# Optimization experiments

Hardware: AMD Instinct MI355X
Metric: run time of the kernel (lower is better)

Reference implementation:

```python
import jax, jax.numpy as jnp
import numpy as np

NUM_CLASSES = 8192
FEAT_DIM = 256
BATCH = 1024
TEMPERATURE = 0.1
BASE_TEMPERATURE = 0.1
PROTO_M = 0.5
EPS = 1e-12  # F.normalize eps


def setup_inputs() -> dict:
    key = jax.random.key(0)
    k1, k2, k3 = jax.random.split(key, 3)
    features = jax.random.normal(k1, (BATCH, FEAT_DIM), dtype=jnp.float32)
    proto = jax.random.normal(k2, (NUM_CLASSES, FEAT_DIM), dtype=jnp.float32)
    # prototypes buffer is unit-normalized after init_class_prototypes
    proto = proto / jnp.maximum(jnp.linalg.norm(proto, axis=1, keepdims=True), EPS)
    labels = jax.random.randint(k3, (BATCH,), 0, NUM_CLASSES, dtype=jnp.int64)
    return {"features": features, "prototypes": proto, "labels": labels}


def _forward(features, prototypes, labels):
    # Sequential per-sample EMA prototype update (order matters for repeated labels)
    def step(proto, fc):
        f, c = fc
        row = proto[c] * PROTO_M + f * (1.0 - PROTO_M)
        row = row / jnp.maximum(jnp.linalg.norm(row), EPS)
        return proto.at[c].set(row), None

    proto, _ = jax.lax.scan(step, prototypes, (features, labels))

    # Pairwise prototype similarity, masked (off-diagonal) mean of exp, then log
    logits = jnp.matmul(proto, proto.T) / TEMPERATURE          # [C, C]
    C = proto.shape[0]
    mask = 1.0 - jnp.eye(C, dtype=logits.dtype)                # zero diagonal
    neg_sum = jnp.sum(mask * jnp.exp(logits), axis=1)          # [C]
    mean_prob_neg = jnp.log(neg_sum / jnp.sum(mask, axis=1))
    # torch drops NaN rows before mean; nanmean reproduces that
    loss = (TEMPERATURE / BASE_TEMPERATURE) * jnp.nanmean(mean_prob_neg)
    return loss


def reference(features, prototypes, labels):
    return _forward(features, prototypes, labels)
```

## Files before the change

kernel.cpp:

```cpp
#include <hip/hip_runtime.h>
#include <hip/hip_bf16.h>
#include <math.h>

#define NUM_CLASSES 8192
#define FEAT_DIM    256
#define BATCH       1024

typedef long fp8x8;
typedef __attribute__((ext_vector_type(4))) float f32x4;

#define GLD16(gp, lp) __builtin_amdgcn_global_load_lds(                       \
    (const __attribute__((address_space(1))) void*)(gp),                      \
    (__attribute__((address_space(3))) void*)(lp), 16, 0, 0)

__global__ __launch_bounds__(1024) void prep_kernel(
    const int* __restrict__ labels, int* __restrict__ offs,
    int* __restrict__ order, float* __restrict__ rowsum) {
  __shared__ int cnt_s[NUM_CLASSES];
  __shared__ int wtot[16];
  const int tid = threadIdx.x;

#pragma unroll
  for (int k = 0; k < NUM_CLASSES / 1024; ++k) {
    cnt_s[k * 1024 + tid] = 0;
    rowsum[k * 1024 + tid] = 0.0f;
  }
  __syncthreads();

  const int lab = labels[tid];
  const int arrival = atomicAdd(&cnt_s[lab], 1);
  __syncthreads();

  const int base = tid * 8;
  int local[8];
  int s = 0;
#pragma unroll
  for (int k = 0; k < 8; ++k) { local[k] = s; s += cnt_s[base + k]; }
  __syncthreads();

  int x = s;
#pragma unroll
  for (int d = 1; d < 64; d <<= 1) {
    int y = __shfl_up(x, d);
    if ((tid & 63) >= d) x += y;
  }
  if ((tid & 63) == 63) wtot[tid >> 6] = x;
  __syncthreads();
  if (tid < 16) {
    int w = wtot[tid];
#pragma unroll
    for (int d = 1; d < 16; d <<= 1) {
      int y = __shfl_up(w, d);
      if (tid >= d) w += y;
    }
    wtot[tid] = w;
  }
  __syncthreads();
  const int wbase = (tid >= 64) ? wtot[(tid >> 6) - 1] : 0;
  const int excl  = wbase + x - s;

#pragma unroll
  for (int k = 0; k < 8; ++k) {
    const int o = excl + local[k];
    cnt_s[base + k] = o;
    offs[base + k]  = o;
  }
  if (tid == 1023) offs[NUM_CLASSES] = BATCH;
  __syncthreads();

  order[cnt_s[lab] + arrival] = tid;
}

__global__ __launch_bounds__(256) void ema_convert_kernel(
    const float* __restrict__ feats, const float* __restrict__ proto,
    const int* __restrict__ offs, const int* __restrict__ order,
    unsigned char* __restrict__ P8) {
  const int c    = (blockIdx.x << 2) + (threadIdx.x >> 6);
  const int lane = threadIdx.x & 63;

  float4 p = ((const float4*)(proto + (size_t)c * FEAT_DIM))[lane];

  const int qs = offs[c], qe = offs[c + 1];
  int prev = -1;
  for (int k = qs; k < qe; ++k) {
    int t = 0x7fffffff;
    for (int q = qs; q < qe; ++q) {
      const int u = order[q];
      if (u > prev && u < t) t = u;
    }
    prev = t;

    float4 f = ((const float4*)(feats + (size_t)t * FEAT_DIM))[lane];
    float4 r;
    r.x = 0.5f * p.x + 0.5f * f.x;
    r.y = 0.5f * p.y + 0.5f * f.y;
    r.z = 0.5f * p.z + 0.5f * f.z;
    r.w = 0.5f * p.w + 0.5f * f.w;
    float ss = r.x * r.x + r.y * r.y + r.z * r.z + r.w * r.w;
#pragma unroll
    for (int off = 32; off; off >>= 1) ss += __shfl_xor(ss, off);
    float inv = 1.0f / fmaxf(sqrtf(ss), 1e-12f);
    p.x = r.x * inv; p.y = r.y * inv; p.z = r.z * inv; p.w = r.w * inv;
  }

  int v = __builtin_amdgcn_cvt_pk_fp8_f32(p.x, p.y, 0, false);
  v = __builtin_amdgcn_cvt_pk_fp8_f32(p.z, p.w, v, true);
  ((int*)(P8 + (size_t)c * FEAT_DIM))[lane] = v;
}

#define BM 128
#define NB (NUM_CLASSES / BM)
#define NTRI (NB * (NB + 1) / 2)
#define NBLK (NTRI / 2)
#define LROW 128

__global__ __launch_bounds__(256, 4) void gemm_rowsum_kernel(
    const unsigned char* __restrict__ P8, float* __restrict__ rowsum) {
  __shared__ __align__(16) char As[BM * LROW];
  __shared__ __align__(16) char Bs[BM * LROW];

  const int hw  = blockIdx.x;
  const int bid = (hw & 7) * (NBLK / 8) + (hw >> 3);

  int rem = bid * 2, bi0 = 0;
  while (rem >= (NB - bi0)) { rem -= (NB - bi0); ++bi0; }
  const int bj0 = bi0 + rem;
  const int bi1 = (bj0 + 1 < NB) ? bi0 : bi0 + 1;
  const int bj1 = (bj0 + 1 < NB) ? bj0 + 1 : bi0 + 1;

  const int tid  = threadIdx.x;
  const int wid  = tid >> 6;
  const int lane = tid & 63;
  const int wm   = wid >> 1;
  const int wn   = wid & 1;

  f32x4 acc[4][4] = {};

  const int rloc = lane >> 3;
  const int csrc = (lane & 7) ^ rloc;
  const unsigned char* PA = P8 + (size_t)(bi0 * BM) * FEAT_DIM;
  const unsigned char* PB = P8 + (size_t)(bj0 * BM) * FEAT_DIM;

#define STAGE(kt)                                                             \
  {                                                                           \
    _Pragma("unroll")                                                         \
    for (int q = 0; q < 4; ++q) {                                             \
      const int L = wid * 4 + q;                                   \
      const int r = L * 8 + rloc;                        \
      const size_t go = (size_t)r * FEAT_DIM + (kt) * 128 + csrc * 16;        \
      GLD16(PA + go, As + L * 1024);                                          \
      GLD16(PB + go, Bs + L * 1024);                                          \
    }                                                                         \
  }

  const int g  = lane >> 4;
  const int rl = lane & 15;

#define COMPUTE()                                                             \
  {                                                                           \
    _Pragma("unroll")                                                         \
    for (int kk = 0; kk < 4; ++kk) {                                          \
      const int cl = 2 * kk + (g >> 1);                \
      const int ib = (g & 1) * 8;                             \
      fp8x8 a[4], b[4];                                                       \
      _Pragma("unroll")                                                       \
      for (int mi = 0; mi < 4; ++mi) {                                        \
        const int row = wm * 64 + mi * 16 + rl;                               \
        a[mi] = *(const fp8x8*)(As + row * LROW + ((cl ^ (row & 7)) << 4) + ib);\
      }                                                                       \
      _Pragma("unroll")                                                       \
      for (int ni = 0; ni < 4; ++ni) {                                        \
        const int row = wn * 64 + ni * 16 + rl;                               \
        b[ni] = *(const fp8x8*)(Bs + row * LROW + ((cl ^ (row & 7)) << 4) + ib);\
      }                                                                       \
      _Pragma("unroll")                                                       \
      for (int mi = 0; mi < 4; ++mi)                                          \
        _Pragma("unroll")                                                     \
        for (int ni = 0; ni < 4; ++ni)                                        \
          acc[mi][ni] = __builtin_amdgcn_mfma_f32_16x16x32_fp8_fp8(           \
              a[mi], b[ni], acc[mi][ni], 0, 0, 0);                            \
    }                                                                         \
  }

#define EPILOGUE(BI, BJ)                                                      \
  {                                                                           \
    const bool diag = ((BI) == (BJ));                                         \
    float col[4] = {0.0f, 0.0f, 0.0f, 0.0f};                                  \
    _Pragma("unroll")                                                         \
    for (int mi = 0; mi < 4; ++mi) {                                          \
      const int growb = (BI) * BM + wm * 64 + mi * 16 + g * 4;                \
      _Pragma("unroll")                                                       \
      for (int v = 0; v < 4; ++v) {                                           \
        const int grow = growb + v;                                           \
        float rs = 0.0f;                                                      \
        _Pragma("unroll")                                                     \
        for (int ni = 0; ni < 4; ++ni) {                                      \
          const int gcol = (BJ) * BM + wn * 64 + ni * 16 + rl;                \
          float e = __expf(10.0f * acc[mi][ni][v]);                           \
          if (diag && grow == gcol) e = 0.0f;                                 \
          rs += e;                                                            \
          col[ni] += e;                                                       \
        }                                                                     \
        rs += __shfl_xor(rs, 1);                                              \
        rs += __shfl_xor(rs, 2);                                              \
        rs += __shfl_xor(rs, 4);                                              \
        rs += __shfl_xor(rs, 8);                                              \
        if (rl == 0) atomicAdd(&rowsum[grow], rs);                            \
      }                                                                       \
    }                                                                         \
    if (!diag) {                                                              \
      _Pragma("unroll")                                                       \
      for (int ni = 0; ni < 4; ++ni) {                                        \
        float cs = col[ni];                                                   \
        cs += __shfl_xor(cs, 16);                                             \
        cs += __shfl_xor(cs, 32);                                             \
        if (g == 0) {                                                         \
          const int gcol = (BJ) * BM + wn * 64 + ni * 16 + rl;                \
          atomicAdd(&rowsum[gcol], cs);                                       \
        }                                                                     \
      }                                                                       \
    }                                                                         \
  }

  STAGE(0);
  __syncthreads();

#pragma unroll
  for (int p = 0; p < 4; ++p) {
    COMPUTE();
    __syncthreads();
    if (p < 3) {
      if (p == 1) {
        PA = P8 + (size_t)(bi1 * BM) * FEAT_DIM;
        PB = P8 + (size_t)(bj1 * BM) * FEAT_DIM;
        STAGE(0);
        EPILOGUE(bi0, bj0);
#pragma unroll
        for (int mi = 0; mi < 4; ++mi)
#pragma unroll
          for (int ni = 0; ni < 4; ++ni)
            acc[mi][ni] = (f32x4){0.0f, 0.0f, 0.0f, 0.0f};
      } else {
        STAGE(1);
      }
      __syncthreads();
    }
  }

  EPILOGUE(bi1, bj1);
}

__global__ __launch_bounds__(256) void finalize_kernel(
    const float* __restrict__ rowsum, float* __restrict__ out) {
  const int tid = threadIdx.x;
  float s = 0.0f;
  for (int i = tid; i < NUM_CLASSES; i += 256) {
    s += logf(rowsum[i] * (1.0f / (float)(NUM_CLASSES - 1)));
  }
#pragma unroll
  for (int off = 32; off; off >>= 1) s += __shfl_xor(s, off);
  __shared__ float red[4];
  if ((tid & 63) == 0) red[tid >> 6] = s;
  __syncthreads();
  if (tid == 0)
    out[0] = (red[0] + red[1] + red[2] + red[3]) * (1.0f / (float)NUM_CLASSES);
}

extern "C" void kernel_launch(void* const* d_in, const int* in_sizes, int n_in,
                              void* d_out, int out_size, void* d_ws, size_t ws_size,
                              hipStream_t stream) {
  const float* feats  = (const float*)d_in[0];
  const float* proto  = (const float*)d_in[1];
  const int*   labels = (const int*)d_in[2];
  float*       out    = (float*)d_out;

  char* ws = (char*)d_ws;
  unsigned char* P8 = (unsigned char*)ws;
  size_t off = (size_t)NUM_CLASSES * FEAT_DIM;
  float* rowsum = (float*)(ws + off);   off += (size_t)NUM_CLASSES * 4;
  int*   offs   = (int*)(ws + off);     off += (size_t)(NUM_CLASSES + 1) * 4;
  int*   order  = (int*)(ws + off);

  prep_kernel<<<1, 1024, 0, stream>>>(labels, offs, order, rowsum);
  ema_convert_kernel<<<NUM_CLASSES / 4, 256, 0, stream>>>(feats, proto, offs,
                                                          order, P8);
  gemm_rowsum_kernel<<<NBLK, 256, 0, stream>>>(P8, rowsum);
  finalize_kernel<<<1, 256, 0, stream>>>(rowsum, out);
}
```

Measured before the change: 62.39 us.

## Drop label-sort prep kernel and double-buffer GEMM over four tiles per block

The single-block prep kernel that bucketed labels by class is removed. Each EMA block now loads all labels into LDS, builds per-lane match bitmasks and walks them in ascending sample order with ballot/ffs, which keeps the sequential update order without the sort. The same kernel also zeroes rowsum. The GEMM now handles four triangular tiles per block with a double-buffered LDS pipeline using explicit vmcnt waits, so global loads overlap compute and epilogues. In exchange it uses twice the LDS and drops the occupancy hint from 4 to 2, and every EMA block rescans all 1024 labels.

```diff
diff --git a/kernel.cpp b/kernel.cpp
--- a/kernel.cpp
+++ b/kernel.cpp
@@ -13,94 +13,57 @@
     (const __attribute__((address_space(1))) void*)(gp),                      \
     (__attribute__((address_space(3))) void*)(lp), 16, 0, 0)
 
-__global__ __launch_bounds__(1024) void prep_kernel(
-    const int* __restrict__ labels, int* __restrict__ offs,
-    int* __restrict__ order, float* __restrict__ rowsum) {
-  __shared__ int cnt_s[NUM_CLASSES];
-  __shared__ int wtot[16];
-  const int tid = threadIdx.x;
-
-#pragma unroll
-  for (int k = 0; k < NUM_CLASSES / 1024; ++k) {
-    cnt_s[k * 1024 + tid] = 0;
-    rowsum[k * 1024 + tid] = 0.0f;
-  }
-  __syncthreads();
-
-  const int lab = labels[tid];
-  const int arrival = atomicAdd(&cnt_s[lab], 1);
-  __syncthreads();
-
-  const int base = tid * 8;
-  int local[8];
-  int s = 0;
-#pragma unroll
-  for (int k = 0; k < 8; ++k) { local[k] = s; s += cnt_s[base + k]; }
-  __syncthreads();
-
-  int x = s;
-#pragma unroll
-  for (int d = 1; d < 64; d <<= 1) {
-    int y = __shfl_up(x, d);
-    if ((tid & 63) >= d) x += y;
-  }
-  if ((tid & 63) == 63) wtot[tid >> 6] = x;
-  __syncthreads();
-  if (tid < 16) {
-    int w = wtot[tid];
-#pragma unroll
-    for (int d = 1; d < 16; d <<= 1) {
-      int y = __shfl_up(w, d);
-      if (tid >= d) w += y;
-    }
-    wtot[tid] = w;
-  }
-  __syncthreads();
-  const int wbase = (tid >= 64) ? wtot[(tid >> 6) - 1] : 0;
-  const int excl  = wbase + x - s;
-
-#pragma unroll
-  for (int k = 0; k < 8; ++k) {
-    const int o = excl + local[k];
-    cnt_s[base + k] = o;
-    offs[base + k]  = o;
-  }
-  if (tid == 1023) offs[NUM_CLASSES] = BATCH;
-  __syncthreads();
-
-  order[cnt_s[lab] + arrival] = tid;
-}
-
 __global__ __launch_bounds__(256) void ema_convert_kernel(
     const float* __restrict__ feats, const float* __restrict__ proto,
-    const int* __restrict__ offs, const int* __restrict__ order,
-    unsigned char* __restrict__ P8) {
-  const int c    = (blockIdx.x << 2) + (threadIdx.x >> 6);
-  const int lane = threadIdx.x & 63;
+    const int* __restrict__ labels, unsigned char* __restrict__ P8,
+    float* __restrict__ rowsum) {
+  __shared__ int lab_s[BATCH];
+  const int tid = threadIdx.x;
+
+  ((int4*)lab_s)[tid] = ((const int4*)labels)[tid];
+  if (blockIdx.x < 32) rowsum[blockIdx.x * 256 + tid] = 0.0f;
+  __syncthreads();
+
+  const int c    = (blockIdx.x << 2) + (tid >> 6);
+  const int lane = tid & 63;
 
   float4 p = ((const float4*)(proto + (size_t)c * FEAT_DIM))[lane];
 
-  const int qs = offs[c], qe = offs[c + 1];
-  int prev = -1;
-  for (int k = qs; k < qe; ++k) {
-    int t = 0x7fffffff;
-    for (int q = qs; q < qe; ++q) {
-      const int u = order[q];
-      if (u > prev && u < t) t = u;
+  const int4 L0 = ((const int4*)lab_s)[lane * 4 + 0];
+  const int4 L1 = ((const int4*)lab_s)[lane * 4 + 1];
+  const int4 L2 = ((const int4*)lab_s)[lane * 4 + 2];
+  const int4 L3 = ((const int4*)lab_s)[lane * 4 + 3];
+  unsigned m = 0;
+  m |= (L0.x == c) << 0;  m |= (L0.y == c) << 1;
+  m |= (L0.z == c) << 2;  m |= (L0.w == c) << 3;
+  m |= (L1.x == c) << 4;  m |= (L1.y == c) << 5;
+  m |= (L1.z == c) << 6;  m |= (L1.w == c) << 7;
+  m |= (L2.x == c) << 8;  m |= (L2.y == c) << 9;
+  m |= (L2.z == c) << 10; m |= (L2.w == c) << 11;
+  m |= (L3.x == c) << 12; m |= (L3.y == c) << 13;
+  m |= (L3.z == c) << 14; m |= (L3.w == c) << 15;
+
+  unsigned long long wm = __ballot(m != 0);
+  while (wm) {
+    const int src = __ffsll((long long)wm) - 1;
+    unsigned mm = __shfl(m, src);
+    while (mm) {
+      const int j = __ffs(mm) - 1;
+      mm &= mm - 1;
+      const int t = src * 16 + j;
+      float4 f = ((const float4*)(feats + (size_t)t * FEAT_DIM))[lane];
+      float4 r;
+      r.x = 0.5f * p.x + 0.5f * f.x;
+      r.y = 0.5f * p.y + 0.5f * f.y;
+      r.z = 0.5f * p.z + 0.5f * f.z;
+      r.w = 0.5f * p.w + 0.5f * f.w;
+      float ss = r.x * r.x + r.y * r.y + r.z * r.z + r.w * r.w;
+#pragma unroll
+      for (int off = 32; off; off >>= 1) ss += __shfl_xor(ss, off);
+      float inv = 1.0f / fmaxf(sqrtf(ss), 1e-12f);
+      p.x = r.x * inv; p.y = r.y * inv; p.z = r.z * inv; p.w = r.w * inv;
     }
-    prev = t;
-
-    float4 f = ((const float4*)(feats + (size_t)t * FEAT_DIM))[lane];
-    float4 r;
-    r.x = 0.5f * p.x + 0.5f * f.x;
-    r.y = 0.5f * p.y + 0.5f * f.y;
-    r.z = 0.5f * p.z + 0.5f * f.z;
-    r.w = 0.5f * p.w + 0.5f * f.w;
-    float ss = r.x * r.x + r.y * r.y + r.z * r.z + r.w * r.w;
-#pragma unroll
-    for (int off = 32; off; off >>= 1) ss += __shfl_xor(ss, off);
-    float inv = 1.0f / fmaxf(sqrtf(ss), 1e-12f);
-    p.x = r.x * inv; p.y = r.y * inv; p.z = r.z * inv; p.w = r.w * inv;
+    wm &= wm - 1;
   }
 
   int v = __builtin_amdgcn_cvt_pk_fp8_f32(p.x, p.y, 0, false);
@@ -111,22 +74,32 @@
 #define BM 128
 #define NB (NUM_CLASSES / BM)
 #define NTRI (NB * (NB + 1) / 2)
-#define NBLK (NTRI / 2)
+#define NBLK (NTRI / 4)
 #define LROW 128
 
-__global__ __launch_bounds__(256, 4) void gemm_rowsum_kernel(
+#define WAITV(N)                                                              \
+  { asm volatile("s_waitcnt vmcnt(" #N ")" ::: "memory");                     \
+    __builtin_amdgcn_sched_barrier(0); }
+#define BAR() __builtin_amdgcn_s_barrier()
+
+__global__ __launch_bounds__(256, 2) void gemm_rowsum_kernel(
     const unsigned char* __restrict__ P8, float* __restrict__ rowsum) {
-  __shared__ __align__(16) char As[BM * LROW];
-  __shared__ __align__(16) char Bs[BM * LROW];
+  __shared__ __align__(16) char lds[2][2][BM * LROW];
 
   const int hw  = blockIdx.x;
   const int bid = (hw & 7) * (NBLK / 8) + (hw >> 3);
 
-  int rem = bid * 2, bi0 = 0;
-  while (rem >= (NB - bi0)) { rem -= (NB - bi0); ++bi0; }
-  const int bj0 = bi0 + rem;
-  const int bi1 = (bj0 + 1 < NB) ? bi0 : bi0 + 1;
-  const int bj1 = (bj0 + 1 < NB) ? bj0 + 1 : bi0 + 1;
+  int bi_[4], bj_[4];
+  {
+    int rem = bid * 4, bi = 0;
+    while (rem >= (NB - bi)) { rem -= (NB - bi); ++bi; }
+    int bj = bi + rem;
+#pragma unroll
+    for (int k = 0; k < 4; ++k) {
+      bi_[k] = bi; bj_[k] = bj;
+      if (bj + 1 < NB) ++bj; else { ++bi; bj = bi; }
+    }
+  }
 
   const int tid  = threadIdx.x;
   const int wid  = tid >> 6;
@@ -138,26 +111,28 @@
 
   const int rloc = lane >> 3;
   const int csrc = (lane & 7) ^ rloc;
-  const unsigned char* PA = P8 + (size_t)(bi0 * BM) * FEAT_DIM;
-  const unsigned char* PB = P8 + (size_t)(bj0 * BM) * FEAT_DIM;
-
-#define STAGE(kt)                                                             \
-  {                                                                           \
+
+#define STAGE(T, KT, BUF)                                                     \
+  {                                                                           \
+    const unsigned char* PA_ = P8 + (size_t)(bi_[T] * BM) * FEAT_DIM;         \
+    const unsigned char* PB_ = P8 + (size_t)(bj_[T] * BM) * FEAT_DIM;         \
     _Pragma("unroll")                                                         \
     for (int q = 0; q < 4; ++q) {                                             \
       const int L = wid * 4 + q;                                   \
       const int r = L * 8 + rloc;                        \
-      const size_t go = (size_t)r * FEAT_DIM + (kt) * 128 + csrc * 16;        \
-      GLD16(PA + go, As + L * 1024);                                          \
-      GLD16(PB + go, Bs + L * 1024);                                          \
+      const size_t go = (size_t)r * FEAT_DIM + (KT) * 128 + csrc * 16;        \
+      GLD16(PA_ + go, &lds[BUF][0][L * 1024]);                                \
+      GLD16(PB_ + go, &lds[BUF][1][L * 1024]);                                \
     }                                                                         \
   }
 
   const int g  = lane >> 4;
   const int rl = lane & 15;
 
-#define COMPUTE()                                                             \
-  {                                                                           \
+#define COMPUTE(BUF)                                                          \
+  {                                                                           \
+    const char* As = &lds[BUF][0][0];                                         \
+    const char* Bs = &lds[BUF][1][0];                                         \
     _Pragma("unroll")                                                         \
     for (int kk = 0; kk < 4; ++kk) {                                          \
       const int cl = 2 * kk + (g >> 1);                \
@@ -182,20 +157,21 @@
     }                                                                         \
   }
 
-#define EPILOGUE(BI, BJ)                                                      \
-  {                                                                           \
-    const bool diag = ((BI) == (BJ));                                         \
+#define EPILOGUE(T)                                                           \
+  {                                                                           \
+    const int BI = bi_[T], BJ = bj_[T];                                       \
+    const bool diag = (BI == BJ);                                             \
     float col[4] = {0.0f, 0.0f, 0.0f, 0.0f};                                  \
     _Pragma("unroll")                                                         \
     for (int mi = 0; mi < 4; ++mi) {                                          \
-      const int growb = (BI) * BM + wm * 64 + mi * 16 + g * 4;                \
+      const int growb = BI * BM + wm * 64 + mi * 16 + g * 4;                  \
       _Pragma("unroll")                                                       \
       for (int v = 0; v < 4; ++v) {                                           \
         const int grow = growb + v;                                           \
         float rs = 0.0f;                                                      \
         _Pragma("unroll")                                                     \
         for (int ni = 0; ni < 4; ++ni) {                                      \
-          const int gcol = (BJ) * BM + wn * 64 + ni * 16 + rl;                \
+          const int gcol = BJ * BM + wn * 64 + ni * 16 + rl;                  \
           float e = __expf(10.0f * acc[mi][ni][v]);                           \
           if (diag && grow == gcol) e = 0.0f;                                 \
           rs += e;                                                            \
@@ -215,39 +191,32 @@
         cs += __shfl_xor(cs, 16);                                             \
         cs += __shfl_xor(cs, 32);                                             \
         if (g == 0) {                                                         \
-          const int gcol = (BJ) * BM + wn * 64 + ni * 16 + rl;                \
+          const int gcol = BJ * BM + wn * 64 + ni * 16 + rl;                  \
           atomicAdd(&rowsum[gcol], cs);                                       \
         }                                                                     \
       }                                                                       \
     }                                                                         \
   }
 
-  STAGE(0);
-  __syncthreads();
-
-#pragma unroll
-  for (int p = 0; p < 4; ++p) {
-    COMPUTE();
-    __syncthreads();
-    if (p < 3) {
-      if (p == 1) {
-        PA = P8 + (size_t)(bi1 * BM) * FEAT_DIM;
-        PB = P8 + (size_t)(bj1 * BM) * FEAT_DIM;
-        STAGE(0);
-        EPILOGUE(bi0, bj0);
-#pragma unroll
-        for (int mi = 0; mi < 4; ++mi)
-#pragma unroll
-          for (int ni = 0; ni < 4; ++ni)
-            acc[mi][ni] = (f32x4){0.0f, 0.0f, 0.0f, 0.0f};
-      } else {
-        STAGE(1);
-      }
-      __syncthreads();
-    }
-  }
-
-  EPILOGUE(bi1, bj1);
+#define ZEROACC()                                                             \
+  {                                                                           \
+    _Pragma("unroll")                                                         \
+    for (int mi = 0; mi < 4; ++mi)                                            \
+      _Pragma("unroll")                                                       \
+      for (int ni = 0; ni < 4; ++ni)                                          \
+        acc[mi][ni] = (f32x4){0.0f, 0.0f, 0.0f, 0.0f};                        \
+  }
+
+  STAGE(0, 0, 0);
+  STAGE(0, 1, 1);
+  WAITV(8); BAR(); COMPUTE(0);              BAR(); STAGE(1, 0, 0);
+  WAITV(8); BAR(); COMPUTE(1); EPILOGUE(0); ZEROACC(); BAR(); STAGE(1, 1, 1);
+  WAITV(8); BAR(); COMPUTE(0);              BAR(); STAGE(2, 0, 0);
+  WAITV(8); BAR(); COMPUTE(1); EPILOGUE(1); ZEROACC(); BAR(); STAGE(2, 1, 1);
+  WAITV(8); BAR(); COMPUTE(0);              BAR(); STAGE(3, 0, 0);
+  WAITV(8); BAR(); COMPUTE(1); EPILOGUE(2); ZEROACC(); BAR(); STAGE(3, 1, 1);
+  WAITV(8); BAR(); COMPUTE(0);              BAR();
+  WAITV(0); BAR(); COMPUTE(1); EPILOGUE(3);
 }
 
 __global__ __launch_bounds__(256) void finalize_kernel(
@@ -276,14 +245,10 @@
 
   char* ws = (char*)d_ws;
   unsigned char* P8 = (unsigned char*)ws;
-  size_t off = (size_t)NUM_CLASSES * FEAT_DIM;
-  float* rowsum = (float*)(ws + off);   off += (size_t)NUM_CLASSES * 4;
-  int*   offs   = (int*)(ws + off);     off += (size_t)(NUM_CLASSES + 1) * 4;
-  int*   order  = (int*)(ws + off);
-
-  prep_kernel<<<1, 1024, 0, stream>>>(labels, offs, order, rowsum);
-  ema_convert_kernel<<<NUM_CLASSES / 4, 256, 0, stream>>>(feats, proto, offs,
-                                                          order, P8);
+  float* rowsum = (float*)(ws + (size_t)NUM_CLASSES * FEAT_DIM);
+
+  ema_convert_kernel<<<NUM_CLASSES / 4, 256, 0, stream>>>(feats, proto, labels,
+                                                          P8, rowsum);
   gemm_rowsum_kernel<<<NBLK, 256, 0, stream>>>(P8, rowsum);
   finalize_kernel<<<1, 256, 0, stream>>>(rowsum, out);
 }
```

Result: slower. 68.94 us (+10.5%).
